# Kernel tuning notes

Hardware: AMD Instinct MI355X
Metric: run time of the kernel (lower is better)

The kernel has to match this reference:

```python
import jax, jax.numpy as jnp
import numpy as np

DIM = 1024
HEADS = 16
DIM_HEAD = 64
INNER = HEADS * DIM_HEAD  # 1024
SCALE = DIM_HEAD ** -0.5


def setup_inputs() -> dict:
    key = jax.random.key(0)
    k1, k2, k3, k4 = jax.random.split(key, 4)
    B, N = 2, 2048
    x = jax.random.normal(k1, (B, N, DIM), dtype=jnp.float32)
    # to_qkv: Linear(dim, 3*inner_dim, bias=False); weight stored as [out, in] in torch,
    # here as [in, out] for x @ W.
    w_qkv = jax.random.normal(k2, (DIM, 3 * INNER), dtype=jnp.float32) * (DIM ** -0.5)
    # to_out: Linear(inner_dim, dim) with bias
    w_out = jax.random.normal(k3, (INNER, DIM), dtype=jnp.float32) * (INNER ** -0.5)
    b_out = jax.random.normal(k4, (DIM,), dtype=jnp.float32) * 0.02
    return {"x": x, "w_qkv": w_qkv, "w_out": w_out, "b_out": b_out}


def reference(x, w_qkv, w_out, b_out):
    B, N, _ = x.shape
    qkv = x @ w_qkv                                  # [B, N, 3*INNER]
    q, k, v = jnp.split(qkv, 3, axis=-1)             # each [B, N, INNER]
    def to_heads(t):
        return t.reshape(B, N, HEADS, DIM_HEAD).transpose(0, 2, 1, 3)  # [B,H,N,D]
    q, k, v = to_heads(q), to_heads(k), to_heads(v)
    dots = jnp.einsum('bhnd,bhmd->bhnm', q, k) * SCALE  # [B,H,N,N]
    attn = jax.nn.softmax(dots, axis=-1)
    out = jnp.einsum('bhnm,bhmd->bhnd', attn, v)        # [B,H,N,D]
    out = out.transpose(0, 2, 1, 3).reshape(B, N, INNER)
    return out @ w_out + b_out
```

## Files before the change

kernel.cpp:

```cpp
#include <hip/hip_runtime.h>
#include <hip/hip_bf16.h>
#include <stdint.h>

#define PDIM   1024
#define HEADS  16
#define DHEAD  64
#define BATCH  2
#define SEQ    2048
#define ROWS   (BATCH*SEQ)
#define NBH    (BATCH*HEADS)

typedef __attribute__((ext_vector_type(8))) short s8v;
typedef __attribute__((ext_vector_type(4))) float f32x4;
typedef unsigned short ushort_t;
typedef unsigned int   uint32;

#define QSCALE 0.18033688011112042f
#define MFIX 12.0f

__device__ __forceinline__ ushort_t f2bf(float x){
  union { float f; uint32 u; } v; v.f = x;
  uint32 r = v.u + 0x7FFFu + ((v.u >> 16) & 1u);
  return (ushort_t)(r >> 16);
}
__device__ __forceinline__ uint32 cvt_pk_bf16(float lo, float hi){
  uint32 r;
  asm("v_cvt_pk_bf16_f32 %0, %1, %2" : "=v"(r) : "v"(lo), "v"(hi));
  return r;
}

typedef const __attribute__((address_space(1))) void* gas_ptr;
typedef __attribute__((address_space(3))) void*       las_ptr;
__device__ __forceinline__ void g2l16(const void* g, void* l){
  __builtin_amdgcn_global_load_lds((gas_ptr)g, (las_ptr)l, 16, 0, 0);
}

__global__ __launch_bounds__(256) void k_prep(
    const float* __restrict__ x, const float* __restrict__ w_qkv,
    const float* __restrict__ w_out,
    ushort_t* __restrict__ Xh, ushort_t* __restrict__ Wqt_h,
    ushort_t* __restrict__ Wot_h){
  __shared__ float tile[64][65];
  const int bid = blockIdx.x;
  if (bid < 4096){
    int i = bid * 256 + threadIdx.x;
    float4 v = reinterpret_cast<const float4*>(x)[i];
    reinterpret_cast<ushort4*>(Xh)[i] =
        make_ushort4(f2bf(v.x), f2bf(v.y), f2bf(v.z), f2bf(v.w));
    return;
  }
  const float* src; ushort_t* dst; int R, C, cb, rb;
  if (bid < 4864){
    int t = bid - 4096; src = w_qkv; dst = Wqt_h; R = 1024; C = 3072;
    cb = (t % 48) * 64; rb = (t / 48) * 64;
  } else {
    int t = bid - 4864; src = w_out; dst = Wot_h; R = 1024; C = 1024;
    cb = (t % 16) * 64; rb = (t / 16) * 64;
  }
  int t = threadIdx.x;
  int lw = t >> 6, lc = t & 63;
#pragma unroll
  for (int i = 0; i < 16; i++){
    int r = i * 4 + lw;
    tile[r][lc] = src[(size_t)(rb + r) * C + cb + lc];
  }
  __syncthreads();
#pragma unroll
  for (int i = 0; i < 16; i++){
    int c = i * 4 + lw;
    dst[(size_t)(cb + c) * R + rb + lc] = f2bf(tile[lc][c]);
  }
}

#define GBM 128
#define GBN 128
#define GBK 64

__global__ __launch_bounds__(256, 2) void k_gemm_qkv(
    const ushort_t* __restrict__ Xh, const ushort_t* __restrict__ Wqt_h,
    ushort_t* __restrict__ Qh, ushort_t* __restrict__ Kh, ushort_t* __restrict__ Vth){
  __shared__ __align__(16) ushort_t Asm[2][GBM * GBK];
  __shared__ __align__(16) ushort_t Bsm[2][GBM * GBK];
  const int tid  = threadIdx.x;
  const int wave = tid >> 6, lane = tid & 63;
  const int mb = blockIdx.y * GBM, nb = blockIdx.x * GBN;
  const int wr = wave >> 1, wc = wave & 1;
  const int l15 = lane & 15, l4 = lane >> 4;
  const int rsub = lane >> 3;
  const int schunk = ((lane & 7) ^ rsub) * 8;
  f32x4 acc[4][4] = {};

  auto stage = [&](int buf, int kb){
    int k0 = kb * GBK;
#pragma unroll
    for (int i = 0; i < 4; i++){
      int row = (i * 4 + wave) * 8 + rsub;
      g2l16(Xh    + (size_t)(mb + row) * 1024 + k0 + schunk, &Asm[buf][(i * 4 + wave) * 512]);
      g2l16(Wqt_h + (size_t)(nb + row) * 1024 + k0 + schunk, &Bsm[buf][(i * 4 + wave) * 512]);
    }
  };

  stage(0, 0);

  for (int kb = 0; kb < 16; kb++){
    const int cur = kb & 1;
    if (kb < 15){
      stage(cur ^ 1, kb + 1);
      asm volatile("s_waitcnt vmcnt(8)" ::: "memory");
    } else {
      asm volatile("s_waitcnt vmcnt(0)" ::: "memory");
    }
    __builtin_amdgcn_s_barrier();
    __builtin_amdgcn_s_setprio(1);
#pragma unroll
    for (int ks = 0; ks < 2; ks++){
      s8v af[4], bfr[4];
#pragma unroll
      for (int f = 0; f < 4; f++){
        int ch = (((ks * 4 + l4) ^ (l15 & 7)) << 3);
        af[f]  = *reinterpret_cast<const s8v*>(&Asm[cur][(wr * 64 + f * 16 + l15) * 64 + ch]);
        bfr[f] = *reinterpret_cast<const s8v*>(&Bsm[cur][(wc * 64 + f * 16 + l15) * 64 + ch]);
      }
#pragma unroll
      for (int fr = 0; fr < 4; fr++)
#pragma unroll
        for (int fc = 0; fc < 4; fc++)
          acc[fr][fc] = __builtin_amdgcn_mfma_f32_16x16x32_bf16(af[fr], bfr[fc], acc[fr][fc], 0, 0, 0);
    }
    __builtin_amdgcn_s_setprio(0);
    __builtin_amdgcn_s_barrier();
  }

  const int pnum = nb >> 10;
#pragma unroll
  for (int fr = 0; fr < 4; fr++){
    int row  = mb + wr * 64 + fr * 16 + l4 * 4;
    int b    = row >> 11;
    int nseq = row & 2047;
#pragma unroll
    for (int fc = 0; fc < 4; fc++){
      int col = nb + wc * 64 + fc * 16 + l15;
      int rem = col & 1023;
      int h = rem >> 6, d = rem & 63;
      int bh = b * 16 + h;
      if (pnum == 0){
        size_t base = ((size_t)bh * SEQ + nseq) * 64 + d;
#pragma unroll
        for (int r = 0; r < 4; r++)
          Qh[base + (size_t)r * 64] = f2bf(acc[fr][fc][r] * QSCALE);
      } else if (pnum == 1){
        size_t base = ((size_t)bh * SEQ + nseq) * 64 + d;
#pragma unroll
        for (int r = 0; r < 4; r++)
          Kh[base + (size_t)r * 64] = f2bf(acc[fr][fc][r]);
      } else {
        size_t base = ((size_t)bh * 64 + d) * SEQ + nseq;
        *reinterpret_cast<ushort4*>(&Vth[base]) =
            make_ushort4(f2bf(acc[fr][fc][0]), f2bf(acc[fr][fc][1]),
                         f2bf(acc[fr][fc][2]), f2bf(acc[fr][fc][3]));
      }
    }
  }
}

__global__ __launch_bounds__(256, 2) void k_gemm_out(
    const ushort_t* __restrict__ Ah, const ushort_t* __restrict__ Bth,
    float* __restrict__ C, const float* __restrict__ bias){
  __shared__ __align__(16) ushort_t Asm[2][GBM * GBK];
  __shared__ __align__(16) ushort_t Bsm[2][GBM * GBK];
  const int tid  = threadIdx.x;
  const int wave = tid >> 6, lane = tid & 63;
  const int mb = blockIdx.y * GBM, nb = blockIdx.x * GBN;
  const int wr = wave >> 1, wc = wave & 1;
  const int l15 = lane & 15, l4 = lane >> 4;
  const int rsub = lane >> 3;
  const int schunk = ((lane & 7) ^ rsub) * 8;
  f32x4 acc[4][4] = {};

  auto stage = [&](int buf, int kb){
    int k0 = kb * GBK;
#pragma unroll
    for (int i = 0; i < 4; i++){
      int row = (i * 4 + wave) * 8 + rsub;
      g2l16(Ah  + (size_t)(mb + row) * 1024 + k0 + schunk, &Asm[buf][(i * 4 + wave) * 512]);
      g2l16(Bth + (size_t)(nb + row) * 1024 + k0 + schunk, &Bsm[buf][(i * 4 + wave) * 512]);
    }
  };

  stage(0, 0);

  for (int kb = 0; kb < 16; kb++){
    const int cur = kb & 1;
    if (kb < 15){
      stage(cur ^ 1, kb + 1);
      asm volatile("s_waitcnt vmcnt(8)" ::: "memory");
    } else {
      asm volatile("s_waitcnt vmcnt(0)" ::: "memory");
    }
    __builtin_amdgcn_s_barrier();
    __builtin_amdgcn_s_setprio(1);
#pragma unroll
    for (int ks = 0; ks < 2; ks++){
      s8v af[4], bfr[4];
#pragma unroll
      for (int f = 0; f < 4; f++){
        int ch = (((ks * 4 + l4) ^ (l15 & 7)) << 3);
        af[f]  = *reinterpret_cast<const s8v*>(&Asm[cur][(wr * 64 + f * 16 + l15) * 64 + ch]);
        bfr[f] = *reinterpret_cast<const s8v*>(&Bsm[cur][(wc * 64 + f * 16 + l15) * 64 + ch]);
      }
#pragma unroll
      for (int fr = 0; fr < 4; fr++)
#pragma unroll
        for (int fc = 0; fc < 4; fc++)
          acc[fr][fc] = __builtin_amdgcn_mfma_f32_16x16x32_bf16(af[fr], bfr[fc], acc[fr][fc], 0, 0, 0);
    }
    __builtin_amdgcn_s_setprio(0);
    __builtin_amdgcn_s_barrier();
  }
#pragma unroll
  for (int fr = 0; fr < 4; fr++){
    int row = mb + wr * 64 + fr * 16 + l4 * 4;
#pragma unroll
    for (int fc = 0; fc < 4; fc++){
      int col = nb + wc * 64 + fc * 16 + l15;
      float bv = bias[col];
#pragma unroll
      for (int r = 0; r < 4; r++)
        C[(size_t)(row + r) * 1024 + col] = acc[fr][fc][r] + bv;
    }
  }
}

__global__ __launch_bounds__(256, 2) void k_flash(
    const ushort_t* __restrict__ Qh, const ushort_t* __restrict__ Kh,
    const ushort_t* __restrict__ Vth, ushort_t* __restrict__ Ah){
  __shared__ __align__(16) ushort_t KhS[2][64 * 64];
  __shared__ __align__(16) ushort_t VhS[2][64 * 64];
  __shared__ __align__(16) ushort_t PhS[128 * 64];
  const int lid = blockIdx.x;
  const int xcd = lid & 7, g = lid >> 3;
  const int bh = xcd * 4 + (g & 3);
  const int qb = (g >> 2) * 128;
  const int tid = threadIdx.x, wave = tid >> 6, lane = tid & 63;
  const int l15 = lane & 15, l4 = lane >> 4;
  const int b = bh >> 4, h = bh & 15;
  const size_t hbase = (size_t)bh * SEQ * 64;
  const int rsub = lane >> 3;
  const int schunk = ((lane & 7) ^ rsub) * 8;

  s8v qhf[2][2];
#pragma unroll
  for (int fr = 0; fr < 2; fr++)
#pragma unroll
    for (int ks = 0; ks < 2; ks++){
      size_t off = hbase + (size_t)(qb + wave * 32 + fr * 16 + l15) * 64 + ks * 32 + l4 * 8;
      qhf[fr][ks] = *reinterpret_cast<const s8v*>(&Qh[off]);
    }

  f32x4 o[2][4] = {};
  float lsum[2] = {0.f, 0.f};

  auto stage = [&](int buf, int kt){
    int kvb = kt * 64;
#pragma unroll
    for (int i = 0; i < 2; i++){
      int row = (i * 4 + wave) * 8 + rsub;
      g2l16(Kh  + hbase + (size_t)(kvb + row) * 64 + schunk, &KhS[buf][(i * 4 + wave) * 512]);
      g2l16(Vth + ((size_t)bh * 64 + row) * SEQ + kvb + schunk, &VhS[buf][(i * 4 + wave) * 512]);
    }
  };

  stage(0, 0);

  for (int kt = 0; kt < 32; kt++){
    const int cur = kt & 1;
    if (kt < 31){
      stage(cur ^ 1, kt + 1);
      asm volatile("s_waitcnt vmcnt(4)" ::: "memory");
    } else {
      asm volatile("s_waitcnt vmcnt(0)" ::: "memory");
    }
    __builtin_amdgcn_s_barrier();

    f32x4 s[2][4] = {};
    __builtin_amdgcn_s_setprio(1);
#pragma unroll
    for (int ks = 0; ks < 2; ks++)
#pragma unroll
      for (int fc = 0; fc < 4; fc++){
        int rK = fc * 16 + l15;
        int ch = ((ks * 4 + l4) ^ (rK & 7)) << 3;
        s8v kh = *reinterpret_cast<const s8v*>(&KhS[cur][rK * 64 + ch]);
        s[0][fc] = __builtin_amdgcn_mfma_f32_16x16x32_bf16(kh, qhf[0][ks], s[0][fc], 0, 0, 0);
        s[1][fc] = __builtin_amdgcn_mfma_f32_16x16x32_bf16(kh, qhf[1][ks], s[1][fc], 0, 0, 0);
      }
    __builtin_amdgcn_s_setprio(0);

#pragma unroll
    for (int fr = 0; fr < 2; fr++){
      int q = wave * 32 + fr * 16 + l15;
      int key = q & 7;
      int base = q * 64;
#pragma unroll
      for (int fc = 0; fc < 4; fc++){
        float p0 = __builtin_amdgcn_exp2f(s[fr][fc][0] - MFIX);
        float p1 = __builtin_amdgcn_exp2f(s[fr][fc][1] - MFIX);
        float p2 = __builtin_amdgcn_exp2f(s[fr][fc][2] - MFIX);
        float p3 = __builtin_amdgcn_exp2f(s[fr][fc][3] - MFIX);
        lsum[fr] += (p0 + p1) + (p2 + p3);
        uint2 w;
        w.x = cvt_pk_bf16(p0, p1);
        w.y = cvt_pk_bf16(p2, p3);
        *reinterpret_cast<uint2*>(
            &PhS[base + (((2 * fc + (l4 >> 1)) ^ key) << 3) + ((l4 & 1) << 2)]) = w;
      }
    }

    __builtin_amdgcn_s_setprio(1);
#pragma unroll
    for (int c = 0; c < 2; c++){
      s8v pa[2];
#pragma unroll
      for (int fr = 0; fr < 2; fr++){
        int q = wave * 32 + fr * 16 + l15;
        pa[fr] = *reinterpret_cast<const s8v*>(&PhS[q * 64 + (((c * 4 + l4) ^ (q & 7)) << 3)]);
      }
#pragma unroll
      for (int fd = 0; fd < 4; fd++){
        int rV = fd * 16 + l15;
        int ch = ((c * 4 + l4) ^ (rV & 7)) << 3;
        s8v vh = *reinterpret_cast<const s8v*>(&VhS[cur][rV * 64 + ch]);
        o[0][fd] = __builtin_amdgcn_mfma_f32_16x16x32_bf16(pa[0], vh, o[0][fd], 0, 0, 0);
        o[1][fd] = __builtin_amdgcn_mfma_f32_16x16x32_bf16(pa[1], vh, o[1][fd], 0, 0, 0);
      }
    }
    __builtin_amdgcn_s_setprio(0);
    __builtin_amdgcn_s_barrier();
  }

#pragma unroll
  for (int fr = 0; fr < 2; fr++){
    lsum[fr] += __shfl_xor(lsum[fr], 16);
    lsum[fr] += __shfl_xor(lsum[fr], 32);
#pragma unroll
    for (int r = 0; r < 4; r++){
      float inv = 1.f / __shfl(lsum[fr], l4 * 4 + r);
      int n = qb + wave * 32 + fr * 16 + l4 * 4 + r;
      size_t rowbase = (size_t)(b * SEQ + n) * 1024 + h * 64;
#pragma unroll
      for (int fd = 0; fd < 4; fd++)
        Ah[rowbase + fd * 16 + l15] = f2bf(o[fr][fd][r] * inv);
    }
  }
}

extern "C" void kernel_launch(void* const* d_in, const int* in_sizes, int n_in,
                              void* d_out, int out_size, void* d_ws, size_t ws_size,
                              hipStream_t stream){
  const float* x     = (const float*)d_in[0];
  const float* w_qkv = (const float*)d_in[1];
  const float* w_out = (const float*)d_in[2];
  const float* b_out = (const float*)d_in[3];
  float* out = (float*)d_out;
  char* ws = (char*)d_ws;

  ushort_t* Xh    = (ushort_t*)(ws);
  ushort_t* Wqt_h = (ushort_t*)(ws + 8388608);
  ushort_t* Wot_h = (ushort_t*)(ws + 14680064);
  ushort_t* Qh    = (ushort_t*)(ws + 16777216);
  ushort_t* Kh    = (ushort_t*)(ws + 25165824);
  ushort_t* Vth   = (ushort_t*)(ws + 33554432);
  ushort_t* Ah    = (ushort_t*)(ws + 41943040);

  k_prep<<<5120, 256, 0, stream>>>(x, w_qkv, w_out, Xh, Wqt_h, Wot_h);
  k_gemm_qkv<<<dim3(24, 32), 256, 0, stream>>>(Xh, Wqt_h, Qh, Kh, Vth);
  k_flash<<<512, 256, 0, stream>>>(Qh, Kh, Vth, Ah);
  k_gemm_out<<<dim3(8, 32), 256, 0, stream>>>(Ah, Wot_h, out, b_out);
}
```

Baseline: 115.7 us.

## Split flash attention over KV halves and combine partials in a separate kernel

The flash kernel now splits the 32 KV tiles into two halves, doubling the grid to 1024 blocks. Each block writes unnormalized fp32 partial outputs and row sums, and a new combine kernel adds them, normalizes, and writes the bf16 attention output. Because a fixed softmax max is used, the partial sums combine without rescaling. V staging is reduced to a single buffer with an extra wait and barrier, and launch bounds are raised to 4 blocks per CU to raise occupancy. The cost is extra fp32 traffic for the partials, one more launch, and less overlap of the V loads.

```diff
diff --git a/kernel.cpp b/kernel.cpp
--- a/kernel.cpp
+++ b/kernel.cpp
@@ -231,19 +231,21 @@
   }
 }
 
-__global__ __launch_bounds__(256, 2) void k_flash(
+__global__ __launch_bounds__(256, 4) void k_flash(
     const ushort_t* __restrict__ Qh, const ushort_t* __restrict__ Kh,
-    const ushort_t* __restrict__ Vth, ushort_t* __restrict__ Ah){
+    const ushort_t* __restrict__ Vth, float* __restrict__ Of, float* __restrict__ Lf){
   __shared__ __align__(16) ushort_t KhS[2][64 * 64];
-  __shared__ __align__(16) ushort_t VhS[2][64 * 64];
+  __shared__ __align__(16) ushort_t VhS[64 * 64];
   __shared__ __align__(16) ushort_t PhS[128 * 64];
   const int lid = blockIdx.x;
   const int xcd = lid & 7, g = lid >> 3;
   const int bh = xcd * 4 + (g & 3);
-  const int qb = (g >> 2) * 128;
+  const int qs = g >> 2;
+  const int qb = (qs & 15) * 128;
+  const int sp = qs >> 4;
+  const int kt0 = sp * 16;
   const int tid = threadIdx.x, wave = tid >> 6, lane = tid & 63;
   const int l15 = lane & 15, l4 = lane >> 4;
-  const int b = bh >> 4, h = bh & 15;
   const size_t hbase = (size_t)bh * SEQ * 64;
   const int rsub = lane >> 3;
   const int schunk = ((lane & 7) ^ rsub) * 8;
@@ -260,25 +262,34 @@
   f32x4 o[2][4] = {};
   float lsum[2] = {0.f, 0.f};
 
-  auto stage = [&](int buf, int kt){
+  auto stageK = [&](int buf, int kt){
     int kvb = kt * 64;
 #pragma unroll
     for (int i = 0; i < 2; i++){
       int row = (i * 4 + wave) * 8 + rsub;
-      g2l16(Kh  + hbase + (size_t)(kvb + row) * 64 + schunk, &KhS[buf][(i * 4 + wave) * 512]);
-      g2l16(Vth + ((size_t)bh * 64 + row) * SEQ + kvb + schunk, &VhS[buf][(i * 4 + wave) * 512]);
+      g2l16(Kh + hbase + (size_t)(kvb + row) * 64 + schunk, &KhS[buf][(i * 4 + wave) * 512]);
     }
   };
-
-  stage(0, 0);
-
-  for (int kt = 0; kt < 32; kt++){
-    const int cur = kt & 1;
-    if (kt < 31){
-      stage(cur ^ 1, kt + 1);
+  auto stageV = [&](int kt){
+    int kvb = kt * 64;
+#pragma unroll
+    for (int i = 0; i < 2; i++){
+      int row = (i * 4 + wave) * 8 + rsub;
+      g2l16(Vth + ((size_t)bh * 64 + row) * SEQ + kvb + schunk, &VhS[(i * 4 + wave) * 512]);
+    }
+  };
+
+  stageK(0, kt0);
+
+  for (int i = 0; i < 16; i++){
+    const int kt = kt0 + i;
+    const int cur = i & 1;
+    stageV(kt);
+    if (i < 15){
+      stageK(cur ^ 1, kt + 1);
       asm volatile("s_waitcnt vmcnt(4)" ::: "memory");
     } else {
-      asm volatile("s_waitcnt vmcnt(0)" ::: "memory");
+      asm volatile("s_waitcnt vmcnt(2)" ::: "memory");
     }
     __builtin_amdgcn_s_barrier();
 
@@ -316,6 +327,13 @@
       }
     }
 
+    if (i < 15){
+      asm volatile("s_waitcnt vmcnt(2)" ::: "memory");
+    } else {
+      asm volatile("s_waitcnt vmcnt(0)" ::: "memory");
+    }
+    __builtin_amdgcn_s_barrier();
+
     __builtin_amdgcn_s_setprio(1);
 #pragma unroll
     for (int c = 0; c < 2; c++){
@@ -329,7 +347,7 @@
       for (int fd = 0; fd < 4; fd++){
         int rV = fd * 16 + l15;
         int ch = ((c * 4 + l4) ^ (rV & 7)) << 3;
-        s8v vh = *reinterpret_cast<const s8v*>(&VhS[cur][rV * 64 + ch]);
+        s8v vh = *reinterpret_cast<const s8v*>(&VhS[rV * 64 + ch]);
         o[0][fd] = __builtin_amdgcn_mfma_f32_16x16x32_bf16(pa[0], vh, o[0][fd], 0, 0, 0);
         o[1][fd] = __builtin_amdgcn_mfma_f32_16x16x32_bf16(pa[1], vh, o[1][fd], 0, 0, 0);
       }
@@ -338,20 +356,42 @@
     __builtin_amdgcn_s_barrier();
   }
 
+  const size_t obase = (size_t)(sp * 32 + bh) * 2048;
 #pragma unroll
   for (int fr = 0; fr < 2; fr++){
     lsum[fr] += __shfl_xor(lsum[fr], 16);
     lsum[fr] += __shfl_xor(lsum[fr], 32);
+    if (l4 == 0)
+      Lf[obase + qb + wave * 32 + fr * 16 + l15] = lsum[fr];
 #pragma unroll
     for (int r = 0; r < 4; r++){
-      float inv = 1.f / __shfl(lsum[fr], l4 * 4 + r);
       int n = qb + wave * 32 + fr * 16 + l4 * 4 + r;
-      size_t rowbase = (size_t)(b * SEQ + n) * 1024 + h * 64;
+      size_t rowbase = (obase + n) * 64;
 #pragma unroll
       for (int fd = 0; fd < 4; fd++)
-        Ah[rowbase + fd * 16 + l15] = f2bf(o[fr][fd][r] * inv);
-    }
-  }
+        Of[rowbase + fd * 16 + l15] = o[fr][fd][r];
+    }
+  }
+}
+
+__global__ __launch_bounds__(256) void k_comb(
+    const float* __restrict__ Of, const float* __restrict__ Lf,
+    ushort_t* __restrict__ Ah){
+  const int bid = blockIdx.x;
+  const int bh = bid >> 7;
+  const int idx = (bid & 127) * 256 + threadIdx.x;
+  const int q = idx >> 4;
+  const int dd = (idx & 15) << 2;
+  const size_t base = ((size_t)bh * 2048 + q) * 64 + dd;
+  float4 a0 = *reinterpret_cast<const float4*>(&Of[base]);
+  float4 a1 = *reinterpret_cast<const float4*>(&Of[base + (size_t)NBH * 2048 * 64]);
+  float L = Lf[(size_t)bh * 2048 + q] + Lf[(size_t)(32 + bh) * 2048 + q];
+  float inv = 1.f / L;
+  int b = bh >> 4, h = bh & 15;
+  size_t orow = ((size_t)(b * 2048 + q)) * 1024 + h * 64 + dd;
+  *reinterpret_cast<ushort4*>(&Ah[orow]) =
+      make_ushort4(f2bf((a0.x + a1.x) * inv), f2bf((a0.y + a1.y) * inv),
+                   f2bf((a0.z + a1.z) * inv), f2bf((a0.w + a1.w) * inv));
 }
 
 extern "C" void kernel_launch(void* const* d_in, const int* in_sizes, int n_in,
@@ -371,9 +411,12 @@
   ushort_t* Kh    = (ushort_t*)(ws + 25165824);
   ushort_t* Vth   = (ushort_t*)(ws + 33554432);
   ushort_t* Ah    = (ushort_t*)(ws + 41943040);
+  float*    Of    = (float*)(ws + 50331648);
+  float*    Lf    = (float*)(ws + 83886080);
 
   k_prep<<<5120, 256, 0, stream>>>(x, w_qkv, w_out, Xh, Wqt_h, Wot_h);
   k_gemm_qkv<<<dim3(24, 32), 256, 0, stream>>>(Xh, Wqt_h, Qh, Kh, Vth);
-  k_flash<<<512, 256, 0, stream>>>(Qh, Kh, Vth, Ah);
+  k_flash<<<1024, 256, 0, stream>>>(Qh, Kh, Vth, Of, Lf);
+  k_comb<<<4096, 256, 0, stream>>>(Of, Lf, Ah);
   k_gemm_out<<<dim3(8, 32), 256, 0, stream>>>(Ah, Wot_h, out, b_out);
 }
```

Measured after the change: 124.4 us. +7.6%, slower.

## Use 128-key tiles with single-buffered K/V staged across QK and PV phases

Applied to the files above, without the earlier changes.

Changes the flash attention loop from 64-key double-buffered K/V tiles to 128-key single-buffered tiles. The K load for the next tile is issued after the QK/softmax phase and the V load after the PV phase, so each transfer overlaps the other half of the iteration. The QK MFMA and exp/bf16 packing are interleaved per key fragment, and the LDS offsets are precomputed. This halves the number of loop iterations and barriers per key element, at the cost of less prefetch distance and larger P and V LDS tiles, which may reduce how many blocks fit on a CU.

```diff
diff --git a/kernel.cpp b/kernel.cpp
--- a/kernel.cpp
+++ b/kernel.cpp
@@ -234,9 +234,9 @@
 __global__ __launch_bounds__(256, 2) void k_flash(
     const ushort_t* __restrict__ Qh, const ushort_t* __restrict__ Kh,
     const ushort_t* __restrict__ Vth, ushort_t* __restrict__ Ah){
-  __shared__ __align__(16) ushort_t KhS[2][64 * 64];
-  __shared__ __align__(16) ushort_t VhS[2][64 * 64];
-  __shared__ __align__(16) ushort_t PhS[128 * 64];
+  __shared__ __align__(16) ushort_t KhS[128 * 64];
+  __shared__ __align__(16) ushort_t VhS[64 * 128];
+  __shared__ __align__(16) ushort_t PhS[128 * 128];
   const int lid = blockIdx.x;
   const int xcd = lid & 7, g = lid >> 3;
   const int bh = xcd * 4 + (g & 3);
@@ -246,7 +246,21 @@
   const int b = bh >> 4, h = bh & 15;
   const size_t hbase = (size_t)bh * SEQ * 64;
   const int rsub = lane >> 3;
-  const int schunk = ((lane & 7) ^ rsub) * 8;
+  const int schunkK = ((lane & 7) ^ rsub) * 8;
+  const int schunkV = ((lane & 15) ^ (wave * 4 + (lane >> 4))) * 8;
+
+  int koff[2], voff[4], proff[4], pwoff[8];
+#pragma unroll
+  for (int ks = 0; ks < 2; ks++)
+    koff[ks] = l15 * 64 + (((ks * 4 + l4) ^ (l15 & 7)) << 3);
+#pragma unroll
+  for (int c = 0; c < 4; c++){
+    voff[c]  = l15 * 128 + (((c * 4 + l4) ^ l15) << 3);
+    proff[c] = (wave * 32 + l15) * 128 + (((c * 4 + l4) ^ l15) << 3);
+  }
+#pragma unroll
+  for (int fc = 0; fc < 8; fc++)
+    pwoff[fc] = (wave * 32 + l15) * 128 + (((fc * 2 + (l4 >> 1)) ^ l15) << 3) + ((l4 & 1) << 2);
 
   s8v qhf[2][2];
 #pragma unroll
@@ -260,82 +274,83 @@
   f32x4 o[2][4] = {};
   float lsum[2] = {0.f, 0.f};
 
-  auto stage = [&](int buf, int kt){
-    int kvb = kt * 64;
-#pragma unroll
-    for (int i = 0; i < 2; i++){
+  auto stageK = [&](int kt){
+    int kvb = kt * 128;
+#pragma unroll
+    for (int i = 0; i < 4; i++){
       int row = (i * 4 + wave) * 8 + rsub;
-      g2l16(Kh  + hbase + (size_t)(kvb + row) * 64 + schunk, &KhS[buf][(i * 4 + wave) * 512]);
-      g2l16(Vth + ((size_t)bh * 64 + row) * SEQ + kvb + schunk, &VhS[buf][(i * 4 + wave) * 512]);
+      g2l16(Kh + hbase + (size_t)(kvb + row) * 64 + schunkK, &KhS[(i * 4 + wave) * 512]);
     }
   };
-
-  stage(0, 0);
-
-  for (int kt = 0; kt < 32; kt++){
-    const int cur = kt & 1;
-    if (kt < 31){
-      stage(cur ^ 1, kt + 1);
-      asm volatile("s_waitcnt vmcnt(4)" ::: "memory");
-    } else {
-      asm volatile("s_waitcnt vmcnt(0)" ::: "memory");
-    }
-    __builtin_amdgcn_s_barrier();
-
-    f32x4 s[2][4] = {};
+  auto stageV = [&](int kt){
+    int kvb = kt * 128;
+#pragma unroll
+    for (int i = 0; i < 4; i++){
+      int d = (i * 4 + wave) * 4 + (lane >> 4);
+      g2l16(Vth + ((size_t)bh * 64 + d) * SEQ + kvb + schunkV, &VhS[(i * 4 + wave) * 512]);
+    }
+  };
+
+  stageK(0);
+  stageV(0);
+
+  for (int i = 0; i < 16; i++){
+    if (i < 15) asm volatile("s_waitcnt vmcnt(4)" ::: "memory");
+    else        asm volatile("s_waitcnt vmcnt(4)" ::: "memory");
+    __builtin_amdgcn_s_barrier();
+
     __builtin_amdgcn_s_setprio(1);
 #pragma unroll
-    for (int ks = 0; ks < 2; ks++)
-#pragma unroll
-      for (int fc = 0; fc < 4; fc++){
-        int rK = fc * 16 + l15;
-        int ch = ((ks * 4 + l4) ^ (rK & 7)) << 3;
-        s8v kh = *reinterpret_cast<const s8v*>(&KhS[cur][rK * 64 + ch]);
-        s[0][fc] = __builtin_amdgcn_mfma_f32_16x16x32_bf16(kh, qhf[0][ks], s[0][fc], 0, 0, 0);
-        s[1][fc] = __builtin_amdgcn_mfma_f32_16x16x32_bf16(kh, qhf[1][ks], s[1][fc], 0, 0, 0);
-      }
+    for (int fc = 0; fc < 8; fc++){
+      s8v kh0 = *reinterpret_cast<const s8v*>(&KhS[koff[0] + fc * 1024]);
+      s8v kh1 = *reinterpret_cast<const s8v*>(&KhS[koff[1] + fc * 1024]);
+      f32x4 t0 = {}, t1 = {};
+      t0 = __builtin_amdgcn_mfma_f32_16x16x32_bf16(kh0, qhf[0][0], t0, 0, 0, 0);
+      t0 = __builtin_amdgcn_mfma_f32_16x16x32_bf16(kh1, qhf[0][1], t0, 0, 0, 0);
+      t1 = __builtin_amdgcn_mfma_f32_16x16x32_bf16(kh0, qhf[1][0], t1, 0, 0, 0);
+      t1 = __builtin_amdgcn_mfma_f32_16x16x32_bf16(kh1, qhf[1][1], t1, 0, 0, 0);
+      {
+        float p0 = __builtin_amdgcn_exp2f(t0[0] - MFIX);
+        float p1 = __builtin_amdgcn_exp2f(t0[1] - MFIX);
+        float p2 = __builtin_amdgcn_exp2f(t0[2] - MFIX);
+        float p3 = __builtin_amdgcn_exp2f(t0[3] - MFIX);
+        lsum[0] += (p0 + p1) + (p2 + p3);
+        uint2 w; w.x = cvt_pk_bf16(p0, p1); w.y = cvt_pk_bf16(p2, p3);
+        *reinterpret_cast<uint2*>(&PhS[pwoff[fc]]) = w;
+      }
+      {
+        float p0 = __builtin_amdgcn_exp2f(t1[0] - MFIX);
+        float p1 = __builtin_amdgcn_exp2f(t1[1] - MFIX);
+        float p2 = __builtin_amdgcn_exp2f(t1[2] - MFIX);
+        float p3 = __builtin_amdgcn_exp2f(t1[3] - MFIX);
+        lsum[1] += (p0 + p1) + (p2 + p3);
+        uint2 w; w.x = cvt_pk_bf16(p0, p1); w.y = cvt_pk_bf16(p2, p3);
+        *reinterpret_cast<uint2*>(&PhS[pwoff[fc] + 2048]) = w;
+      }
+    }
     __builtin_amdgcn_s_setprio(0);
 
-#pragma unroll
-    for (int fr = 0; fr < 2; fr++){
-      int q = wave * 32 + fr * 16 + l15;
-      int key = q & 7;
-      int base = q * 64;
-#pragma unroll
-      for (int fc = 0; fc < 4; fc++){
-        float p0 = __builtin_amdgcn_exp2f(s[fr][fc][0] - MFIX);
-        float p1 = __builtin_amdgcn_exp2f(s[fr][fc][1] - MFIX);
-        float p2 = __builtin_amdgcn_exp2f(s[fr][fc][2] - MFIX);
-        float p3 = __builtin_amdgcn_exp2f(s[fr][fc][3] - MFIX);
-        lsum[fr] += (p0 + p1) + (p2 + p3);
-        uint2 w;
-        w.x = cvt_pk_bf16(p0, p1);
-        w.y = cvt_pk_bf16(p2, p3);
-        *reinterpret_cast<uint2*>(
-            &PhS[base + (((2 * fc + (l4 >> 1)) ^ key) << 3) + ((l4 & 1) << 2)]) = w;
-      }
-    }
+    asm volatile("s_waitcnt vmcnt(0)" ::: "memory");
+    __builtin_amdgcn_s_barrier();
+
+    if (i < 15) stageK(i + 1);
 
     __builtin_amdgcn_s_setprio(1);
 #pragma unroll
-    for (int c = 0; c < 2; c++){
-      s8v pa[2];
-#pragma unroll
-      for (int fr = 0; fr < 2; fr++){
-        int q = wave * 32 + fr * 16 + l15;
-        pa[fr] = *reinterpret_cast<const s8v*>(&PhS[q * 64 + (((c * 4 + l4) ^ (q & 7)) << 3)]);
-      }
+    for (int c = 0; c < 4; c++){
+      s8v pa0 = *reinterpret_cast<const s8v*>(&PhS[proff[c]]);
+      s8v pa1 = *reinterpret_cast<const s8v*>(&PhS[proff[c] + 2048]);
 #pragma unroll
       for (int fd = 0; fd < 4; fd++){
-        int rV = fd * 16 + l15;
-        int ch = ((c * 4 + l4) ^ (rV & 7)) << 3;
-        s8v vh = *reinterpret_cast<const s8v*>(&VhS[cur][rV * 64 + ch]);
-        o[0][fd] = __builtin_amdgcn_mfma_f32_16x16x32_bf16(pa[0], vh, o[0][fd], 0, 0, 0);
-        o[1][fd] = __builtin_amdgcn_mfma_f32_16x16x32_bf16(pa[1], vh, o[1][fd], 0, 0, 0);
+        s8v vh = *reinterpret_cast<const s8v*>(&VhS[voff[c] + fd * 2048]);
+        o[0][fd] = __builtin_amdgcn_mfma_f32_16x16x32_bf16(pa0, vh, o[0][fd], 0, 0, 0);
+        o[1][fd] = __builtin_amdgcn_mfma_f32_16x16x32_bf16(pa1, vh, o[1][fd], 0, 0, 0);
       }
     }
     __builtin_amdgcn_s_setprio(0);
     __builtin_amdgcn_s_barrier();
+
+    if (i < 15) stageV(i + 1);
   }
 
 #pragma unroll
```

New measurement: 118.0 us. +2.0%, slower.

## Switch flash kernel to 32x32x16 MFMA and keep P in registers via permlane swap

Applied to the files above, without the earlier changes.

Rewrites the attention inner loop to use 32x32x16 bf16 MFMA tiles instead of 16x16x32, computing S^T per wave as two 32x32 blocks. The softmax probabilities are packed to bf16 and rearranged across lanes with v_permlane32_swap instead of being written to and re-read from the LDS P buffer. This removes the PhS shared allocation and its LDS round trip and reduces fragment loads per MFMA. The output epilogue and row-sum reduction are adapted to the 32x32 accumulator layout.

```diff
diff --git a/kernel.cpp b/kernel.cpp
--- a/kernel.cpp
+++ b/kernel.cpp
@@ -12,6 +12,7 @@
 
 typedef __attribute__((ext_vector_type(8))) short s8v;
 typedef __attribute__((ext_vector_type(4))) float f32x4;
+typedef __attribute__((ext_vector_type(16))) float f32x16;
 typedef unsigned short ushort_t;
 typedef unsigned int   uint32;
 
@@ -236,29 +237,31 @@
     const ushort_t* __restrict__ Vth, ushort_t* __restrict__ Ah){
   __shared__ __align__(16) ushort_t KhS[2][64 * 64];
   __shared__ __align__(16) ushort_t VhS[2][64 * 64];
-  __shared__ __align__(16) ushort_t PhS[128 * 64];
   const int lid = blockIdx.x;
   const int xcd = lid & 7, g = lid >> 3;
   const int bh = xcd * 4 + (g & 3);
   const int qb = (g >> 2) * 128;
   const int tid = threadIdx.x, wave = tid >> 6, lane = tid & 63;
-  const int l15 = lane & 15, l4 = lane >> 4;
-  const int b = bh >> 4, h = bh & 15;
+  const int l31 = lane & 31, hh = lane >> 5;
+  const int b = bh >> 4, hd = bh & 15;
   const size_t hbase = (size_t)bh * SEQ * 64;
   const int rsub = lane >> 3;
   const int schunk = ((lane & 7) ^ rsub) * 8;
 
-  s8v qhf[2][2];
-#pragma unroll
-  for (int fr = 0; fr < 2; fr++)
-#pragma unroll
-    for (int ks = 0; ks < 2; ks++){
-      size_t off = hbase + (size_t)(qb + wave * 32 + fr * 16 + l15) * 64 + ks * 32 + l4 * 8;
-      qhf[fr][ks] = *reinterpret_cast<const s8v*>(&Qh[off]);
-    }
-
-  f32x4 o[2][4] = {};
-  float lsum[2] = {0.f, 0.f};
+  int fch[4];
+#pragma unroll
+  for (int s = 0; s < 4; s++)
+    fch[s] = (((2 * s + hh) ^ (l31 & 7)) << 3);
+  const int fbase = l31 * 64;
+
+  s8v qf[4];
+#pragma unroll
+  for (int s = 0; s < 4; s++)
+    qf[s] = *reinterpret_cast<const s8v*>(
+        &Qh[hbase + (size_t)(qb + wave * 32 + l31) * 64 + s * 16 + hh * 8]);
+
+  f32x16 o0 = {}, o1 = {};
+  float lsum = 0.f;
 
   auto stage = [&](int buf, int kt){
     int kvb = kt * 64;
@@ -282,75 +285,62 @@
     }
     __builtin_amdgcn_s_barrier();
 
-    f32x4 s[2][4] = {};
+    f32x16 s0 = {}, s1 = {};
     __builtin_amdgcn_s_setprio(1);
 #pragma unroll
-    for (int ks = 0; ks < 2; ks++)
-#pragma unroll
-      for (int fc = 0; fc < 4; fc++){
-        int rK = fc * 16 + l15;
-        int ch = ((ks * 4 + l4) ^ (rK & 7)) << 3;
-        s8v kh = *reinterpret_cast<const s8v*>(&KhS[cur][rK * 64 + ch]);
-        s[0][fc] = __builtin_amdgcn_mfma_f32_16x16x32_bf16(kh, qhf[0][ks], s[0][fc], 0, 0, 0);
-        s[1][fc] = __builtin_amdgcn_mfma_f32_16x16x32_bf16(kh, qhf[1][ks], s[1][fc], 0, 0, 0);
-      }
+    for (int s = 0; s < 4; s++){
+      s8v kf0 = *reinterpret_cast<const s8v*>(&KhS[cur][fbase + fch[s]]);
+      s8v kf1 = *reinterpret_cast<const s8v*>(&KhS[cur][fbase + 2048 + fch[s]]);
+      s0 = __builtin_amdgcn_mfma_f32_32x32x16_bf16(kf0, qf[s], s0, 0, 0, 0);
+      s1 = __builtin_amdgcn_mfma_f32_32x32x16_bf16(kf1, qf[s], s1, 0, 0, 0);
+    }
     __builtin_amdgcn_s_setprio(0);
 
-#pragma unroll
-    for (int fr = 0; fr < 2; fr++){
-      int q = wave * 32 + fr * 16 + l15;
-      int key = q & 7;
-      int base = q * 64;
-#pragma unroll
-      for (int fc = 0; fc < 4; fc++){
-        float p0 = __builtin_amdgcn_exp2f(s[fr][fc][0] - MFIX);
-        float p1 = __builtin_amdgcn_exp2f(s[fr][fc][1] - MFIX);
-        float p2 = __builtin_amdgcn_exp2f(s[fr][fc][2] - MFIX);
-        float p3 = __builtin_amdgcn_exp2f(s[fr][fc][3] - MFIX);
-        lsum[fr] += (p0 + p1) + (p2 + p3);
-        uint2 w;
-        w.x = cvt_pk_bf16(p0, p1);
-        w.y = cvt_pk_bf16(p2, p3);
-        *reinterpret_cast<uint2*>(
-            &PhS[base + (((2 * fc + (l4 >> 1)) ^ key) << 3) + ((l4 & 1) << 2)]) = w;
-      }
+    uint32 w[2][8];
+#pragma unroll
+    for (int t = 0; t < 8; t++){
+      float pa = __builtin_amdgcn_exp2f(s0[2 * t]     - MFIX);
+      float pb = __builtin_amdgcn_exp2f(s0[2 * t + 1] - MFIX);
+      lsum += pa + pb;
+      w[0][t] = cvt_pk_bf16(pa, pb);
+    }
+#pragma unroll
+    for (int t = 0; t < 8; t++){
+      float pa = __builtin_amdgcn_exp2f(s1[2 * t]     - MFIX);
+      float pb = __builtin_amdgcn_exp2f(s1[2 * t + 1] - MFIX);
+      lsum += pa + pb;
+      w[1][t] = cvt_pk_bf16(pa, pb);
     }
 
     __builtin_amdgcn_s_setprio(1);
 #pragma unroll
-    for (int c = 0; c < 2; c++){
-      s8v pa[2];
-#pragma unroll
-      for (int fr = 0; fr < 2; fr++){
-        int q = wave * 32 + fr * 16 + l15;
-        pa[fr] = *reinterpret_cast<const s8v*>(&PhS[q * 64 + (((c * 4 + l4) ^ (q & 7)) << 3)]);
-      }
-#pragma unroll
-      for (int fd = 0; fd < 4; fd++){
-        int rV = fd * 16 + l15;
-        int ch = ((c * 4 + l4) ^ (rV & 7)) << 3;
-        s8v vh = *reinterpret_cast<const s8v*>(&VhS[cur][rV * 64 + ch]);
-        o[0][fd] = __builtin_amdgcn_mfma_f32_16x16x32_bf16(pa[0], vh, o[0][fd], 0, 0, 0);
-        o[1][fd] = __builtin_amdgcn_mfma_f32_16x16x32_bf16(pa[1], vh, o[1][fd], 0, 0, 0);
-      }
+    for (int s = 0; s < 4; s++){
+      const int rb = s >> 1, u = (s & 1) * 4;
+      uint32 m0 = w[rb][u],     m2 = w[rb][u + 2];
+      uint32 m1 = w[rb][u + 1], m3 = w[rb][u + 3];
+      asm("v_permlane32_swap_b32 %0, %1" : "+v"(m0), "+v"(m2));
+      asm("v_permlane32_swap_b32 %0, %1" : "+v"(m1), "+v"(m3));
+      union { uint32 u4[4]; s8v v; } pf;
+      pf.u4[0] = m0; pf.u4[1] = m1; pf.u4[2] = m2; pf.u4[3] = m3;
+      s8v vf0 = *reinterpret_cast<const s8v*>(&VhS[cur][fbase + fch[s]]);
+      s8v vf1 = *reinterpret_cast<const s8v*>(&VhS[cur][fbase + 2048 + fch[s]]);
+      o0 = __builtin_amdgcn_mfma_f32_32x32x16_bf16(pf.v, vf0, o0, 0, 0, 0);
+      o1 = __builtin_amdgcn_mfma_f32_32x32x16_bf16(pf.v, vf1, o1, 0, 0, 0);
     }
     __builtin_amdgcn_s_setprio(0);
     __builtin_amdgcn_s_barrier();
   }
 
-#pragma unroll
-  for (int fr = 0; fr < 2; fr++){
-    lsum[fr] += __shfl_xor(lsum[fr], 16);
-    lsum[fr] += __shfl_xor(lsum[fr], 32);
-#pragma unroll
-    for (int r = 0; r < 4; r++){
-      float inv = 1.f / __shfl(lsum[fr], l4 * 4 + r);
-      int n = qb + wave * 32 + fr * 16 + l4 * 4 + r;
-      size_t rowbase = (size_t)(b * SEQ + n) * 1024 + h * 64;
-#pragma unroll
-      for (int fd = 0; fd < 4; fd++)
-        Ah[rowbase + fd * 16 + l15] = f2bf(o[fr][fd][r] * inv);
-    }
+  lsum += __shfl_xor(lsum, 32);
+  float linv = 1.f / lsum;
+#pragma unroll
+  for (int r = 0; r < 16; r++){
+    int q = (r & 3) + 8 * (r >> 2) + 4 * hh;
+    float sc = __shfl(linv, q);
+    int n = qb + wave * 32 + q;
+    size_t rowb = (size_t)(b * SEQ + n) * 1024 + hd * 64;
+    Ah[rowb + l31]      = f2bf(o0[r] * sc);
+    Ah[rowb + 32 + l31] = f2bf(o1[r] * sc);
   }
 }
 
```

Result: no change. 115.7 us (+0.0%).
